# Performance work log

Measured on AMD Instinct MI355X. Metric: run time of the kernel, lower is better.

Reference implementation:

```python
import jax, jax.numpy as jnp
import numpy as np

NX = 768
N_HEAD = 12
R = 8
SCALING = 16.0  # lora_alpha*r / r = lora_alpha
NEG = 1e10


def setup_inputs() -> dict:
    key = jax.random.key(0)
    ks = jax.random.split(key, 7)
    B, S = 2, 2048
    return {
        "x": jax.random.normal(ks[0], (B, S, NX), dtype=jnp.float32),
        "w_attn": jax.random.normal(ks[1], (NX, 3 * NX), dtype=jnp.float32) * 0.02,
        "b_attn": jax.random.normal(ks[2], (3 * NX,), dtype=jnp.float32) * 0.02,
        "lora_A": jax.random.normal(ks[3], (3 * R, NX), dtype=jnp.float32) * 0.02,
        "lora_B": jax.random.normal(ks[4], (3 * NX, R), dtype=jnp.float32) * 0.02,
        "w_proj": jax.random.normal(ks[5], (NX, NX), dtype=jnp.float32) * 0.02,
        "b_proj": jax.random.normal(ks[6], (NX,), dtype=jnp.float32) * 0.02,
    }


def reference(x, w_attn, b_attn, lora_A, lora_B, w_proj, b_proj):
    B, S, _ = x.shape
    dh = NX // N_HEAD

    # --- LoRA-augmented QKV projection (MergedLinear, fan_in_fan_out=True, unmerged) ---
    qkv = x @ w_attn + b_attn  # [B,S,3*NX]
    A = lora_A.reshape(3, R, NX)          # per-chunk A_i: [r, nx]
    Bm = lora_B.reshape(3, NX, R)         # per-chunk B_i: [nx, r]
    # x @ (B_i @ A_i).T = (x @ A_i.T) @ B_i.T, grouped over q/k/v chunks c
    t = jnp.einsum('bsd,crd->bscr', x, A)           # [B,S,3,r]
    delta = jnp.einsum('bscr,cer->bsce', t, Bm)     # [B,S,3,nx]
    qkv = qkv + delta.reshape(B, S, 3 * NX) * SCALING

    # --- split heads ---
    q, k, v = jnp.split(qkv, 3, axis=-1)
    q = q.reshape(B, S, N_HEAD, dh).transpose(0, 2, 1, 3)  # [B,H,S,dh]
    k = k.reshape(B, S, N_HEAD, dh).transpose(0, 2, 1, 3)  # [B,H,S,dh]
    v = v.reshape(B, S, N_HEAD, dh).transpose(0, 2, 1, 3)  # [B,H,S,dh]

    # --- manual causal softmax attention (scale=True) ---
    w = jnp.einsum('bhqd,bhkd->bhqk', q, k) / jnp.sqrt(jnp.float32(dh))
    mask = jnp.tril(jnp.ones((S, S), dtype=w.dtype))[None, None]  # tril bias buffer
    w = w * mask - NEG * (1.0 - mask)
    w = jax.nn.softmax(w, axis=-1)
    a = jnp.einsum('bhqk,bhkd->bhqd', w, v)  # [B,H,S,dh]

    # --- merge heads + output projection (Conv1D) ---
    a = a.transpose(0, 2, 1, 3).reshape(B, S, NX)
    a = a @ w_proj + b_proj

    present = jnp.stack([k, v])  # [2,B,H,S,dh]
    return a, present
```

## Files before the change

kernel.cpp:

```cpp
#include <hip/hip_runtime.h>
#include <cstdint>

#define NXC 768
#define NHEAD 12
#define BB 2
#define SS 2048
#define MTOT (BB*SS)
#define NQKV (3*NXC)
#define PRESENT_HALF (BB*NHEAD*SS*64)

typedef __bf16 bf16x8 __attribute__((ext_vector_type(8)));
typedef float f32x4 __attribute__((ext_vector_type(4)));
typedef float f32x16 __attribute__((ext_vector_type(16)));

__device__ __forceinline__ uint16_t f2bf(float f) {
    uint32_t u = __builtin_bit_cast(uint32_t, f);
    uint32_t r = (u + 0x7FFFu + ((u >> 16) & 1u)) >> 16;
    return (uint16_t)r;
}

__device__ __forceinline__ bf16x8 vfrag(ushort4 a, ushort4 b) {
    union { bf16x8 v; ushort4 u[2]; } r;
    r.u[0] = a; r.u[1] = b;
    return r.v;
}

__device__ __forceinline__ void gload16(const uint16_t* g, uint16_t* l) {
    __builtin_amdgcn_global_load_lds(
        (const __attribute__((address_space(1))) unsigned int*)g,
        (__attribute__((address_space(3))) unsigned int*)l, 16, 0, 0);
}


__global__ __launch_bounds__(256) void prep_all(
    const float* __restrict__ x, uint16_t* __restrict__ x_bf,
    const float* __restrict__ w_attn, const float* __restrict__ lora_A,
    const float* __restrict__ lora_B, uint16_t* __restrict__ weffT,
    const float* __restrict__ w_proj, uint16_t* __restrict__ wpT) {
    __shared__ float T[64][65];
    __shared__ float Af[8][64];
    __shared__ float Bf[64][8];
    const int t = threadIdx.x;
    const int blk = blockIdx.x;
    if (blk < 3072) {
        int i = blk * 256 + t;
        float4 v = ((const float4*)x)[i];
        ushort4 o;
        o.x = f2bf(v.x); o.y = f2bf(v.y); o.z = f2bf(v.z); o.w = f2bf(v.w);
        ((ushort4*)x_bf)[i] = o;
        return;
    }
    if (blk < 3504) {
        const int i2 = blk - 3072;
        const int n0 = (i2 % 36) * 64, k0 = (i2 / 36) * 64;
        const int c = n0 / NXC;
        {
            const int nn = t & 63, q = t >> 6;
#pragma unroll
            for (int j = 0; j < 16; ++j) {
                int kr = q + j * 4;
                T[kr][nn] = w_attn[(size_t)(k0 + kr) * NQKV + n0 + nn];
            }
        }
        {
            int idx = t;
            Af[idx >> 6][idx & 63] = lora_A[(size_t)(c * 8 + (idx >> 6)) * NXC + k0 + (idx & 63)];
            idx += 256;
            Af[idx >> 6][idx & 63] = lora_A[(size_t)(c * 8 + (idx >> 6)) * NXC + k0 + (idx & 63)];
            Bf[t >> 3][t & 7] = lora_B[(size_t)(n0 + (t >> 3)) * 8 + (t & 7)];
            idx = t + 256;
            Bf[idx >> 3][idx & 7] = lora_B[(size_t)(n0 + (idx >> 3)) * 8 + (idx & 7)];
        }
        __syncthreads();
        const int kk = t & 63, q = t >> 6;
#pragma unroll
        for (int j = 0; j < 16; ++j) {
            int nn = q + j * 4;
            float d = 0.f;
#pragma unroll
            for (int r = 0; r < 8; ++r) d += Af[r][kk] * Bf[nn][r];
            weffT[(size_t)(n0 + nn) * NXC + k0 + kk] = f2bf(T[kk][nn] + 16.0f * d);
        }
        return;
    }
    {
        const int i3 = blk - 3504;
        const int n0 = (i3 % 12) * 64, k0 = (i3 / 12) * 64;
        {
            const int nn = t & 63, q = t >> 6;
#pragma unroll
            for (int j = 0; j < 16; ++j) {
                int kr = q + j * 4;
                T[kr][nn] = w_proj[(size_t)(k0 + kr) * NXC + n0 + nn];
            }
        }
        __syncthreads();
        const int kk = t & 63, q = t >> 6;
#pragma unroll
        for (int j = 0; j < 16; ++j) {
            int nn = q + j * 4;
            wpT[(size_t)(n0 + nn) * NXC + k0 + kk] = f2bf(T[kk][nn]);
        }
    }
}


template<int MODE, int BM, int BN, int NBX>
__global__ __launch_bounds__(256) void gemm_bt(
    const uint16_t* __restrict__ Abf, const uint16_t* __restrict__ BTbf,
    const float* __restrict__ bias, float* __restrict__ outf,
    uint16_t* __restrict__ q_bf, uint16_t* __restrict__ k_bf,
    uint16_t* __restrict__ vT_bf) {
    constexpr int MR = BM / 32;
    constexpr int NR = BN / 32;
    __shared__ uint16_t As[3][BM][32];
    __shared__ uint16_t Bs[3][BN][32];
    const int t = threadIdx.x;
    const int lane = t & 63;
    const int w = t >> 6;
    const int wr = (w >> 1) * (BM / 2);
    const int wc = (w & 1) * (BN / 2);
    const int lr16 = lane & 15;
    const int lk = (lane >> 4) << 3;
    const int id = blockIdx.x;
    const int wgid = (id & 7) * ((int)gridDim.x >> 3) + (id >> 3);
    const int by = wgid / NBX, bx = wgid - by * NBX;
    const size_t arow0 = (size_t)by * BM;
    const size_t brow0 = (size_t)bx * BN;
    const int sr = lane >> 2;
    const int sc = (lane & 3) * 8;
    const uint16_t* Asrc = Abf + (arow0 + w * 16 + sr) * NXC + sc;
    const uint16_t* Bsrc = BTbf + (brow0 + w * 16 + sr) * NXC + sc;

    f32x4 acc[MR][NR];
#pragma unroll
    for (int m = 0; m < MR; ++m)
#pragma unroll
        for (int n = 0; n < NR; ++n) acc[m][n] = (f32x4){0.f, 0.f, 0.f, 0.f};

#define STAGE(buf, k0) do { \
    _Pragma("unroll") \
    for (int i = 0; i < BM / 64; ++i) \
        gload16(Asrc + (size_t)i * 64 * NXC + (k0), &As[buf][i * 64 + w * 16][0]); \
    _Pragma("unroll") \
    for (int i = 0; i < BN / 64; ++i) \
        gload16(Bsrc + (size_t)i * 64 * NXC + (k0), &Bs[buf][i * 64 + w * 16][0]); \
} while (0)

    STAGE(0, 0);
    STAGE(1, 32);

    int cur = 0;
    for (int kt = 0; kt < 24; ++kt) {
        if (kt < 23) asm volatile("s_waitcnt vmcnt(3)" ::: "memory");
        else         asm volatile("s_waitcnt vmcnt(0)" ::: "memory");
        __builtin_amdgcn_s_barrier();
        __builtin_amdgcn_sched_barrier(0);
        if (kt + 2 < 24) {
            int b2 = cur + 2; if (b2 >= 3) b2 -= 3;
            const int k2 = (kt + 2) << 5;
            STAGE(b2, k2);
        }
        bf16x8 af[MR], bv[NR];
#pragma unroll
        for (int m = 0; m < MR; ++m) af[m] = *(const bf16x8*)&As[cur][wr + m * 16 + lr16][lk];
#pragma unroll
        for (int n = 0; n < NR; ++n) bv[n] = *(const bf16x8*)&Bs[cur][wc + n * 16 + lr16][lk];
#pragma unroll
        for (int m = 0; m < MR; ++m)
#pragma unroll
            for (int n = 0; n < NR; ++n)
                acc[m][n] = __builtin_amdgcn_mfma_f32_16x16x32_bf16(af[m], bv[n], acc[m][n], 0, 0, 0);
        cur = (cur == 2) ? 0 : cur + 1;
    }
#undef STAGE

    const int rowb = (lane >> 4) << 2;
    const float QSCALE = 0.125f * 1.44269504f;
#pragma unroll
    for (int m = 0; m < MR; ++m) {
        int grow0 = (int)arow0 + wr + m * 16 + rowb;
#pragma unroll
        for (int n = 0; n < NR; ++n) {
            int gcol = (int)brow0 + wc + n * 16 + lr16;
            float bvs = bias[gcol];
            if (MODE == 1) {
#pragma unroll
                for (int ri = 0; ri < 4; ++ri) {
                    int grow = grow0 + ri;
                    outf[(size_t)grow * NXC + gcol] = acc[m][n][ri] + bvs;
                }
            } else {
                int c = gcol >= 2 * NXC ? 2 : (gcol >= NXC ? 1 : 0);
                int e = gcol - c * NXC;
                int h = e >> 6, d = e & 63;
                int b = grow0 >> 11, s0 = grow0 & 2047;
                if (c == 0) {
#pragma unroll
                    for (int ri = 0; ri < 4; ++ri) {
                        float v = acc[m][n][ri] + bvs;
                        q_bf[((size_t)(b * NHEAD + h) * SS + s0 + ri) * 64 + d] = f2bf(v * QSCALE);
                    }
                } else if (c == 1) {
#pragma unroll
                    for (int ri = 0; ri < 4; ++ri) {
                        float v = acc[m][n][ri] + bvs;
                        size_t hidx = (size_t)(b * NHEAD + h) * SS + s0 + ri;
                        k_bf[hidx * 64 + d] = f2bf(v);
                        outf[hidx * 64 + d] = v;
                    }
                } else {
                    float v0 = acc[m][n][0] + bvs, v1 = acc[m][n][1] + bvs;
                    float v2 = acc[m][n][2] + bvs, v3 = acc[m][n][3] + bvs;
                    ushort4 pv;
                    pv.x = f2bf(v0); pv.y = f2bf(v1); pv.z = f2bf(v2); pv.w = f2bf(v3);
                    *(ushort4*)(vT_bf + ((size_t)(b * NHEAD + h) * 64 + d) * SS + s0) = pv;
                    size_t hb = ((size_t)(b * NHEAD + h) * SS + s0) * 64 + d;
                    outf[PRESENT_HALF + hb] = v0;
                    outf[PRESENT_HALF + hb + 64] = v1;
                    outf[PRESENT_HALF + hb + 128] = v2;
                    outf[PRESENT_HALF + hb + 192] = v3;
                }
            }
        }
    }
}


__global__ __launch_bounds__(256) void attn_kernel(
    const uint16_t* __restrict__ qb, const uint16_t* __restrict__ kb,
    const uint16_t* __restrict__ vtb, uint16_t* __restrict__ ab) {
    __shared__ __align__(16) uint8_t smem[32768];
    uint16_t* KT0 = (uint16_t*)smem;
    uint16_t* VT0 = (uint16_t*)(smem + 16384);
    float* Mlp = (float*)smem;
    float* Llp = Mlp + 64;
    float* Ofp = Llp + 64;

    const int t = threadIdx.x;
    const int w = t >> 6, lane = t & 63;
    const int qw = w & 1, khalf = w >> 1;
    const int l31 = lane & 31, hi = lane >> 5;
    const int i8 = lane >> 3, c8 = lane & 7;
    const int id = blockIdx.x;
    const int xcd = id & 7, slot = id >> 3;
    const int lh = slot % 3, qs = slot / 3;
    const int qi = 31 - qs;
    const int bh = xcd * 3 + lh;
    const int qbase = qi * 64;
    const int q = qbase + qw * 32 + l31;
    const uint16_t* qh = qb + (size_t)bh * (SS * 64);
    const uint16_t* kh = kb + (size_t)bh * (SS * 64);
    const uint16_t* vh = vtb + (size_t)bh * (64 * SS);
    const int nkt = qi + 1;

    bf16x8 qf[4];
#pragma unroll
    for (int dc = 0; dc < 4; ++dc)
        qf[dc] = *(const bf16x8*)(qh + (size_t)q * 64 + dc * 16 + hi * 8);

    f32x16 o0, o1;
#pragma unroll
    for (int i = 0; i < 16; ++i) { o0[i] = 0.f; o1[i] = 0.f; }
    float m_run = -1e30f, l_run = 0.f;

    const uint16_t* ksrc = kh + (size_t)i8 * 64 + ((c8 ^ i8) << 3);
    const uint16_t* vsrc = vh + (size_t)i8 * SS + ((c8 ^ i8) << 3);
    const int j0 = (w & 1) * 4;

    if (khalf == 0) {
#pragma unroll
        for (int j = 0; j < 4; ++j)
            gload16(ksrc + (size_t)((j0 + j) * 8) * 64, KT0 + (j0 + j) * 8 * 64);
    } else {
#pragma unroll
        for (int j = 0; j < 4; ++j)
            gload16(vsrc + (size_t)((j0 + j) * 8) * SS, VT0 + (j0 + j) * 8 * 64);
    }
    asm volatile("s_waitcnt vmcnt(0)" ::: "memory");
    __syncthreads();

    int cur = 0;
    for (int kt = 0; kt < nkt; ++kt) {
        if (kt + 1 < nkt) {
            const int nb = (kt + 1) << 6;
            uint16_t* KTn = KT0 + (cur ^ 1) * 4096;
            uint16_t* VTn = VT0 + (cur ^ 1) * 4096;
            if (khalf == 0) {
#pragma unroll
                for (int j = 0; j < 4; ++j)
                    gload16(ksrc + (size_t)(nb + (j0 + j) * 8) * 64, KTn + (j0 + j) * 8 * 64);
            } else {
#pragma unroll
                for (int j = 0; j < 4; ++j)
                    gload16(vsrc + (size_t)((j0 + j) * 8) * SS + nb, VTn + (j0 + j) * 8 * 64);
            }
        }
        const uint16_t* KTc = KT0 + cur * 4096;
        const uint16_t* VTc = VT0 + cur * 4096;

        f32x16 sa;
#pragma unroll
        for (int i = 0; i < 16; ++i) sa[i] = 0.f;
        const int krow = khalf * 32 + l31;
        __builtin_amdgcn_s_setprio(1);
#pragma unroll
        for (int dc = 0; dc < 4; ++dc) {
            bf16x8 kf = *(const bf16x8*)(KTc + krow * 64 + (((dc * 2 + hi) ^ (l31 & 7)) << 3));
            sa = __builtin_amdgcn_mfma_f32_32x32x16_bf16(kf, qf[dc], sa, 0, 0, 0);
        }
        __builtin_amdgcn_s_setprio(0);
        if (kt == qi) {
            const int qrel = qw * 32 + l31;
#pragma unroll
            for (int r = 0; r < 16; ++r) {
                int key = khalf * 32 + (r & 3) + 8 * (r >> 2) + 4 * hi;
                sa[r] = (key > qrel) ? -1e30f : sa[r];
            }
        }
        float m8[8];
#pragma unroll
        for (int g = 0; g < 8; ++g) m8[g] = fmaxf(sa[g * 2], sa[g * 2 + 1]);
        float lm = fmaxf(fmaxf(fmaxf(m8[0], m8[1]), fmaxf(m8[2], m8[3])),
                         fmaxf(fmaxf(m8[4], m8[5]), fmaxf(m8[6], m8[7])));
        if (__any(lm > m_run + 8.f)) {
            float tmf = fmaxf(lm, __shfl_xor(lm, 32));
            float nm = fmaxf(m_run, tmf);
            float corr = __builtin_amdgcn_exp2f(m_run - nm);
            l_run *= corr;
#pragma unroll
            for (int i = 0; i < 16; ++i) { o0[i] *= corr; o1[i] *= corr; }
            m_run = nm;
        }
        float e[16];
#pragma unroll
        for (int r = 0; r < 16; ++r) e[r] = __builtin_amdgcn_exp2f(sa[r] - m_run);
        bf16x8 pa0, pa1;
#pragma unroll
        for (int r = 0; r < 8; ++r) { pa0[r] = (__bf16)e[r]; pa1[r] = (__bf16)e[8 + r]; }
        l_run += ((e[0] + e[1]) + (e[2] + e[3])) + ((e[4] + e[5]) + (e[6] + e[7]))
               + ((e[8] + e[9]) + (e[10] + e[11])) + ((e[12] + e[13]) + (e[14] + e[15]));
        const int rx = l31 & 7;
        __builtin_amdgcn_s_setprio(1);
#pragma unroll
        for (int dblk = 0; dblk < 2; ++dblk) {
            const uint16_t* vrow = VTc + (dblk * 32 + l31) * 64;
            ushort4 v0 = *(const ushort4*)(vrow + (((khalf * 4 + 0) ^ rx) << 3) + hi * 4);
            ushort4 v1 = *(const ushort4*)(vrow + (((khalf * 4 + 1) ^ rx) << 3) + hi * 4);
            ushort4 v2 = *(const ushort4*)(vrow + (((khalf * 4 + 2) ^ rx) << 3) + hi * 4);
            ushort4 v3 = *(const ushort4*)(vrow + (((khalf * 4 + 3) ^ rx) << 3) + hi * 4);
            f32x16 oo = dblk ? o1 : o0;
            oo = __builtin_amdgcn_mfma_f32_32x32x16_bf16(vfrag(v0, v1), pa0, oo, 0, 0, 0);
            oo = __builtin_amdgcn_mfma_f32_32x32x16_bf16(vfrag(v2, v3), pa1, oo, 0, 0, 0);
            if (dblk) o1 = oo; else o0 = oo;
        }
        __builtin_amdgcn_s_setprio(0);
        asm volatile("s_waitcnt vmcnt(0)" ::: "memory");
        __syncthreads();
        cur ^= 1;
    }

    const float lf = l_run + __shfl_xor(l_run, 32);
    const int qrow = qw * 32 + l31;
    if (khalf == 1) {
        if (hi == 0) { Mlp[qrow] = m_run; Llp[qrow] = lf; }
#pragma unroll
        for (int dblk = 0; dblk < 2; ++dblk)
#pragma unroll
            for (int rg = 0; rg < 4; ++rg) {
                f32x16 oo = dblk ? o1 : o0;
                f32x4 v;
                v[0] = oo[rg * 4 + 0]; v[1] = oo[rg * 4 + 1];
                v[2] = oo[rg * 4 + 2]; v[3] = oo[rg * 4 + 3];
                *(f32x4*)&Ofp[qrow * 68 + dblk * 32 + rg * 8 + hi * 4] = v;
            }
    }
    __syncthreads();
    if (khalf == 0) {
        const float m2 = Mlp[qrow], l2 = Llp[qrow];
        const float ms = fmaxf(m_run, m2);
        const float wA = __builtin_amdgcn_exp2f(m_run - ms);
        const float wB = __builtin_amdgcn_exp2f(m2 - ms);
        const float inv = 1.f / (lf * wA + l2 * wB);
        const int b = bh / NHEAD, h = bh - b * NHEAD;
        uint16_t* abp = ab + ((size_t)(b * SS + q)) * NXC + h * 64;
#pragma unroll
        for (int dblk = 0; dblk < 2; ++dblk)
#pragma unroll
            for (int rg = 0; rg < 4; ++rg) {
                f32x16 oo = dblk ? o1 : o0;
                f32x4 po = *(const f32x4*)&Ofp[qrow * 68 + dblk * 32 + rg * 8 + hi * 4];
                ushort4 wv;
                wv.x = f2bf((oo[rg * 4 + 0] * wA + po[0] * wB) * inv);
                wv.y = f2bf((oo[rg * 4 + 1] * wA + po[1] * wB) * inv);
                wv.z = f2bf((oo[rg * 4 + 2] * wA + po[2] * wB) * inv);
                wv.w = f2bf((oo[rg * 4 + 3] * wA + po[3] * wB) * inv);
                *(ushort4*)(abp + dblk * 32 + rg * 8 + hi * 4) = wv;
            }
    }
}


extern "C" void kernel_launch(void* const* d_in, const int* in_sizes, int n_in,
                              void* d_out, int out_size, void* d_ws, size_t ws_size,
                              hipStream_t stream) {
    const float* x      = (const float*)d_in[0];
    const float* w_attn = (const float*)d_in[1];
    const float* b_attn = (const float*)d_in[2];
    const float* lora_A = (const float*)d_in[3];
    const float* lora_B = (const float*)d_in[4];
    const float* w_proj = (const float*)d_in[5];
    const float* b_proj = (const float*)d_in[6];
    float* out = (float*)d_out;
    float* present = out + (size_t)MTOT * NXC;

    uint16_t* ws    = (uint16_t*)d_ws;
    uint16_t* x_bf  = ws;
    uint16_t* weffT = x_bf + 3145728;
    uint16_t* wpT   = weffT + 1769472;
    uint16_t* q_bf  = wpT + 589824;
    uint16_t* k_bf  = q_bf + 3145728;
    uint16_t* vT_bf = k_bf + 3145728;
    uint16_t* a_bf  = vT_bf + 3145728;

    prep_all<<<dim3(3648), dim3(256), 0, stream>>>(x, x_bf, w_attn, lora_A, lora_B,
                                                   weffT, w_proj, wpT);
    gemm_bt<0, 128, 64, 36><<<dim3(1152), dim3(256), 0, stream>>>(
        x_bf, weffT, b_attn, present, q_bf, k_bf, vT_bf);
    attn_kernel<<<dim3(768), dim3(256), 0, stream>>>(q_bf, k_bf, vT_bf, a_bf);
    gemm_bt<1, 128, 64, 12><<<dim3(384), dim3(256), 0, stream>>>(
        a_bf, wpT, b_proj, out, nullptr, nullptr, nullptr);
}
```

Baseline: 102.2 us.

## Use BK=64 double-buffered GEMM with XOR-swizzled LDS and MFMA priority

Restructures the QKV/proj GEMM mainloop from a 3-stage BK=32 pipeline to a 2-stage BK=64 pipeline, halving the number of barriers per K sweep. LDS tiles are widened to 64 columns and stored with an XOR swizzle on 16-byte chunks to avoid bank conflicts on fragment reads. MFMAs are wrapped in s_setprio to favour the math wave. The cost is less prefetch depth: each iteration waits on its own next-tile loads at the end, so global latency may be less hidden.

Result: faster. 89.59 us (-12.3%).

```diff
diff --git a/kernel.cpp b/kernel.cpp
--- a/kernel.cpp
+++ b/kernel.cpp
@@ -113,24 +113,26 @@
     uint16_t* __restrict__ vT_bf) {
     constexpr int MR = BM / 32;
     constexpr int NR = BN / 32;
-    __shared__ uint16_t As[3][BM][32];
-    __shared__ uint16_t Bs[3][BN][32];
+    constexpr int AI = BM / 32;
+    constexpr int BI = BN / 32;
+    __shared__ uint16_t As[2][BM][64];
+    __shared__ uint16_t Bs[2][BN][64];
     const int t = threadIdx.x;
     const int lane = t & 63;
     const int w = t >> 6;
     const int wr = (w >> 1) * (BM / 2);
     const int wc = (w & 1) * (BN / 2);
     const int lr16 = lane & 15;
-    const int lk = (lane >> 4) << 3;
+    const int hi2 = lane >> 4;
     const int id = blockIdx.x;
     const int wgid = (id & 7) * ((int)gridDim.x >> 3) + (id >> 3);
     const int by = wgid / NBX, bx = wgid - by * NBX;
     const size_t arow0 = (size_t)by * BM;
     const size_t brow0 = (size_t)bx * BN;
-    const int sr = lane >> 2;
-    const int sc = (lane & 3) * 8;
-    const uint16_t* Asrc = Abf + (arow0 + w * 16 + sr) * NXC + sc;
-    const uint16_t* Bsrc = BTbf + (brow0 + w * 16 + sr) * NXC + sc;
+    const int srow = lane >> 3;
+    const int schunk = ((lane & 7) ^ (srow & 7)) << 3;
+    const uint16_t* Asrc = Abf + (arow0 + w * (BM / 4) + srow) * NXC + schunk;
+    const uint16_t* Bsrc = BTbf + (brow0 + w * (BN / 4) + srow) * NXC + schunk;
 
     f32x4 acc[MR][NR];
 #pragma unroll
@@ -140,38 +142,47 @@
 
 #define STAGE(buf, k0) do { \
     _Pragma("unroll") \
-    for (int i = 0; i < BM / 64; ++i) \
-        gload16(Asrc + (size_t)i * 64 * NXC + (k0), &As[buf][i * 64 + w * 16][0]); \
+    for (int j = 0; j < AI; ++j) \
+        gload16(Asrc + (size_t)(j * 8) * NXC + (k0), &As[buf][w * (BM / 4) + j * 8][0]); \
     _Pragma("unroll") \
-    for (int i = 0; i < BN / 64; ++i) \
-        gload16(Bsrc + (size_t)i * 64 * NXC + (k0), &Bs[buf][i * 64 + w * 16][0]); \
+    for (int j = 0; j < BI; ++j) \
+        gload16(Bsrc + (size_t)(j * 8) * NXC + (k0), &Bs[buf][w * (BN / 4) + j * 8][0]); \
 } while (0)
 
     STAGE(0, 0);
-    STAGE(1, 32);
+    asm volatile("s_waitcnt vmcnt(0)" ::: "memory");
+    __builtin_amdgcn_s_barrier();
 
     int cur = 0;
-    for (int kt = 0; kt < 24; ++kt) {
-        if (kt < 23) asm volatile("s_waitcnt vmcnt(3)" ::: "memory");
-        else         asm volatile("s_waitcnt vmcnt(0)" ::: "memory");
+    for (int kt = 0; kt < 12; ++kt) {
+        if (kt + 1 < 12) STAGE(cur ^ 1, (kt + 1) << 6);
+        bf16x8 af[2][MR], bv[2][NR];
+#pragma unroll
+        for (int kk = 0; kk < 2; ++kk) {
+#pragma unroll
+            for (int m = 0; m < MR; ++m) {
+                const int r = wr + m * 16 + lr16;
+                af[kk][m] = *(const bf16x8*)&As[cur][r][(((kk * 4 + hi2) ^ (r & 7)) << 3)];
+            }
+#pragma unroll
+            for (int n = 0; n < NR; ++n) {
+                const int r = wc + n * 16 + lr16;
+                bv[kk][n] = *(const bf16x8*)&Bs[cur][r][(((kk * 4 + hi2) ^ (r & 7)) << 3)];
+            }
+        }
+        __builtin_amdgcn_s_setprio(1);
+#pragma unroll
+        for (int kk = 0; kk < 2; ++kk)
+#pragma unroll
+            for (int m = 0; m < MR; ++m)
+#pragma unroll
+                for (int n = 0; n < NR; ++n)
+                    acc[m][n] = __builtin_amdgcn_mfma_f32_16x16x32_bf16(af[kk][m], bv[kk][n],
+                                                                        acc[m][n], 0, 0, 0);
+        __builtin_amdgcn_s_setprio(0);
+        asm volatile("s_waitcnt vmcnt(0)" ::: "memory");
         __builtin_amdgcn_s_barrier();
-        __builtin_amdgcn_sched_barrier(0);
-        if (kt + 2 < 24) {
-            int b2 = cur + 2; if (b2 >= 3) b2 -= 3;
-            const int k2 = (kt + 2) << 5;
-            STAGE(b2, k2);
-        }
-        bf16x8 af[MR], bv[NR];
-#pragma unroll
-        for (int m = 0; m < MR; ++m) af[m] = *(const bf16x8*)&As[cur][wr + m * 16 + lr16][lk];
-#pragma unroll
-        for (int n = 0; n < NR; ++n) bv[n] = *(const bf16x8*)&Bs[cur][wc + n * 16 + lr16][lk];
-#pragma unroll
-        for (int m = 0; m < MR; ++m)
-#pragma unroll
-            for (int n = 0; n < NR; ++n)
-                acc[m][n] = __builtin_amdgcn_mfma_f32_16x16x32_bf16(af[m], bv[n], acc[m][n], 0, 0, 0);
-        cur = (cur == 2) ? 0 : cur + 1;
+        cur ^= 1;
     }
 #undef STAGE
 
```
